# Kernel optimization log

Hardware: AMD Instinct MI355X
Metric: run time of the kernel (lower is better)

Reference implementation:

```python
import jax, jax.numpy as jnp
import numpy as np

B, S, H, NH, HD = 4, 4096, 1024, 16, 64

def setup_inputs() -> dict:
    key = jax.random.key(0)
    ks = jax.random.split(key, 5)
    scale = 1.0 / np.sqrt(H)
    return {
        "hidden_states": jax.random.normal(ks[0], (B, S, H), dtype=jnp.float32),
        "Wq": jax.random.normal(ks[1], (H, H), dtype=jnp.float32) * scale,
        "Wk": jax.random.normal(ks[2], (H, H), dtype=jnp.float32) * scale,
        "Wv": jax.random.normal(ks[3], (H, H), dtype=jnp.float32) * scale,
        "Wo": jax.random.normal(ks[4], (H, H), dtype=jnp.float32) * scale,
    }

def reference(hidden_states, Wq, Wk, Wv, Wo):
    b, s, h = hidden_states.shape
    # torch nn.Linear: y = x @ W.T
    q = (hidden_states @ Wq.T).reshape(b, s, NH, HD)
    k = (hidden_states @ Wk.T).reshape(b, s, NH, HD)
    v = (hidden_states @ Wv.T).reshape(b, s, NH, HD)
    # feature map: ELU (as in source, no +1)
    q = jax.nn.elu(q)
    k = jax.nn.elu(k)
    # per-head kv state: sum over sequence of outer products k_s v_s^T -> [b,h,d,e]
    kv = jnp.einsum('bshd,bshe->bhde', k, v)
    out = jnp.einsum('bqhd,bhde->bqhe', q, kv)  # [b,s,h,e]
    out = out.reshape(b, s, h)
    return out @ Wo.T  # dropout p=0.0 is identity
```

## Files before the change

### kernel.cpp

```cpp
#include <hip/hip_runtime.h>
#include <cstdint>
#include <cstddef>

#define B_  4
#define S_  4096
#define H_  1024
#define NH_ 16
#define M_  (B_*S_)

typedef __bf16 bf16x8 __attribute__((ext_vector_type(8)));
typedef float  f32x4  __attribute__((ext_vector_type(4)));

__device__ __forceinline__ unsigned short f2b(float f) {
  union { float f; unsigned u; } v; v.f = f;
  unsigned r = v.u + 0x7FFFu + ((v.u >> 16) & 1u);
  return (unsigned short)(r >> 16);
}
__device__ __forceinline__ float b2f(unsigned short u) {
  union { unsigned u; float f; } v; v.u = ((unsigned)u) << 16;
  return v.f;
}

#define GLD16(g, l) __builtin_amdgcn_global_load_lds( \
    (const __attribute__((address_space(1))) void*)(g), \
    (__attribute__((address_space(3))) void*)(l), 16, 0, 0)

#define VM0()  asm volatile("s_waitcnt vmcnt(0)" ::: "memory")
#define VM2()  asm volatile("s_waitcnt vmcnt(2)" ::: "memory")
#define BAR()  do { asm volatile("" ::: "memory"); __builtin_amdgcn_s_barrier(); \
                    asm volatile("" ::: "memory"); } while (0)

__global__ void cast_f32_bf16(const float* __restrict__ src,
                              unsigned short* __restrict__ dst, int n4) {
  int i = blockIdx.x * blockDim.x + threadIdx.x;
  if (i >= n4) return;
  float4 f = reinterpret_cast<const float4*>(src)[i];
  ushort4 o;
  o.x = f2b(f.x); o.y = f2b(f.y); o.z = f2b(f.z); o.w = f2b(f.w);
  reinterpret_cast<ushort4*>(dst)[i] = o;
}

__global__ void cast_w4(const float* __restrict__ w0, const float* __restrict__ w1,
                        const float* __restrict__ w2, const float* __restrict__ w3,
                        unsigned short* __restrict__ dst) {
  int i = blockIdx.x * blockDim.x + threadIdx.x;
  int w = i >> 18, j = i & 0x3FFFF;
  const float* src = (w == 0) ? w0 : (w == 1) ? w1 : (w == 2) ? w2 : w3;
  float4 f = reinterpret_cast<const float4*>(src)[j];
  ushort4 o;
  o.x = f2b(f.x); o.y = f2b(f.y); o.z = f2b(f.z); o.w = f2b(f.w);
  reinterpret_cast<ushort4*>(dst)[i] = o;
}

template<int MODE>
__global__ __launch_bounds__(512, 2) void gemm256(
    const unsigned short* __restrict__ A_,
    const unsigned short* __restrict__ Bt_,
    void* __restrict__ out) {
  __shared__ __align__(16) unsigned short LDS[2][2][16384];

  const int NTN = (MODE == 0) ? 12 : 4;
  const int nx  = gridDim.x >> 3;
  const int b2  = (blockIdx.x & 7) * nx + (blockIdx.x >> 3);
  const int tileM = (b2 / NTN) << 8;
  const int tileN = (b2 % NTN) << 8;

  const unsigned short* Bt_e =
      (MODE == 1) ? (Bt_ + ((size_t)(tileM >> 12) << 20)) : Bt_;

  const int tid  = threadIdx.x;
  const int lane = tid & 63, wv = tid >> 6;
  const int wmi  = wv >> 2;
  const int wni  = wv & 3;
  const int fr   = lane & 15, fq = lane >> 4;

  const int sr0 = tid >> 3,          sc0 = (tid & 7) ^ (sr0 & 7);
  const int sr1 = (tid + 512) >> 3,  sc1 = (tid & 7) ^ (sr1 & 7);

#define STG(NB, ARR, HM, SRC, RB, TT) do {                                      \
    GLD16((SRC) + (size_t)((RB) + (HM)*128 + sr0) * 1024 + (TT)*64 + sc0*8,     \
          &LDS[NB][ARR][(HM)*8192 + wv*512]);                                   \
    GLD16((SRC) + (size_t)((RB) + (HM)*128 + sr1) * 1024 + (TT)*64 + sc1*8,     \
          &LDS[NB][ARR][(HM)*8192 + 4096 + wv*512]);                            \
  } while (0)

#define READA(CB, MQ, DST) do {                                                 \
    _Pragma("unroll")                                                           \
    for (int m = 0; m < 4; m++) {                                               \
      int r = (MQ)*128 + wmi*64 + m*16 + fr;                                    \
      DST[m][0] = *(const bf16x8*)&LDS[CB][0][r*64 + ((fq    ) ^ (r&7))*8];     \
      DST[m][1] = *(const bf16x8*)&LDS[CB][0][r*64 + ((4 + fq) ^ (r&7))*8];     \
    }                                                                           \
  } while (0)

#define READB(CB, NQ, DST) do {                                                 \
    _Pragma("unroll")                                                           \
    for (int n = 0; n < 2; n++) {                                               \
      int r = (NQ)*128 + wni*32 + n*16 + fr;                                    \
      DST[n][0] = *(const bf16x8*)&LDS[CB][1][r*64 + ((fq    ) ^ (r&7))*8];     \
      DST[n][1] = *(const bf16x8*)&LDS[CB][1][r*64 + ((4 + fq) ^ (r&7))*8];     \
    }                                                                           \
  } while (0)

#define MMQ(MQ, NQ, AS, BS) do {                                                \
    __builtin_amdgcn_s_setprio(1);                                              \
    _Pragma("unroll")                                                           \
    for (int m = 0; m < 4; m++)                                                 \
      _Pragma("unroll")                                                         \
      for (int n = 0; n < 2; n++) {                                             \
        acc[MQ][NQ][m][n] = __builtin_amdgcn_mfma_f32_16x16x32_bf16(            \
            AS[m][0], BS[n][0], acc[MQ][NQ][m][n], 0, 0, 0);                    \
        acc[MQ][NQ][m][n] = __builtin_amdgcn_mfma_f32_16x16x32_bf16(            \
            AS[m][1], BS[n][1], acc[MQ][NQ][m][n], 0, 0, 0);                    \
      }                                                                         \
    __builtin_amdgcn_s_setprio(0);                                              \
  } while (0)

  f32x4 zero = {0.f, 0.f, 0.f, 0.f};
  f32x4 acc[2][2][4][2];
#pragma unroll
  for (int a = 0; a < 2; a++)
#pragma unroll
    for (int b = 0; b < 2; b++)
#pragma unroll
      for (int m = 0; m < 4; m++)
#pragma unroll
        for (int n = 0; n < 2; n++) acc[a][b][m][n] = zero;

  bf16x8 aA[4][2], aB[4][2], bA[2][2], bB[2][2];

  STG(0, 0, 0, A_,   tileM, 0);
  STG(0, 1, 0, Bt_e, tileN, 0);
  STG(0, 1, 1, Bt_e, tileN, 0);
  STG(0, 0, 1, A_,   tileM, 0);
  VM0();
  BAR();
  READA(0, 0, aA); READB(0, 0, bA);

  int cb = 0;
#pragma unroll 1
  for (int t = 0; t < 15; ++t) {
    const int nb = cb ^ 1;
    READB(cb, 1, bB);
    STG(nb, 0, 0, A_,   tileM, t + 1);
    VM2(); BAR();
    MMQ(0, 0, aA, bA);
    READA(cb, 1, aB);
    STG(nb, 1, 0, Bt_e, tileN, t + 1);
    BAR();
    MMQ(0, 1, aA, bB);
    STG(nb, 1, 1, Bt_e, tileN, t + 1);
    BAR();
    MMQ(1, 1, aB, bB);
    STG(nb, 0, 1, A_,   tileM, t + 1);
    VM2(); BAR();
    MMQ(1, 0, aB, bA);
    READA(nb, 0, aA); READB(nb, 0, bA);
    cb = nb;
  }
  READB(cb, 1, bB); VM0(); BAR();
  MMQ(0, 0, aA, bA);
  READA(cb, 1, aB); BAR();
  MMQ(0, 1, aA, bB);
  BAR();
  MMQ(1, 1, aB, bB);
  BAR();
  MMQ(1, 0, aB, bA);

  if (MODE == 0) {
    unsigned short* Ep = &LDS[0][0][0];
    const int reg = tileN >> 10;
    const bool doELU = (reg < 2);
    BAR();
#pragma unroll
    for (int mq = 0; mq < 2; mq++)
#pragma unroll
      for (int nq = 0; nq < 2; nq++)
#pragma unroll
        for (int m = 0; m < 4; m++)
#pragma unroll
          for (int n = 0; n < 2; n++)
#pragma unroll
            for (int r = 0; r < 4; r++) {
              int row = mq * 128 + wmi * 64 + m * 16 + fq * 4 + r;
              int col = nq * 128 + wni * 32 + n * 16 + fr;
              float v = acc[mq][nq][m][n][r];
              if (doELU) v = v > 0.f ? v : (expf(v) - 1.f);
              Ep[row * 256 + (col ^ ((row & 7) << 3))] = f2b(v);
            }
    BAR();
    unsigned short* outp = (unsigned short*)out + (size_t)reg * M_ * H_;
    const int lcbase = tileN & 1023;
#pragma unroll
    for (int it = 0; it < 16; it++) {
      int g = it * 512 + tid;
      int row = g >> 5, col = (g & 31) * 8;
      bf16x8 val = *(const bf16x8*)&Ep[row * 256 + (col ^ ((row & 7) << 3))];
      *(bf16x8*)&outp[(size_t)(tileM + row) * H_ + lcbase + col] = val;
    }
  } else {
    float* Ef = (float*)&LDS[0][0][0];
#pragma unroll
    for (int mq = 0; mq < 2; mq++) {
      BAR();
#pragma unroll
      for (int nq = 0; nq < 2; nq++)
#pragma unroll
        for (int m = 0; m < 4; m++)
#pragma unroll
          for (int n = 0; n < 2; n++)
#pragma unroll
            for (int r = 0; r < 4; r++) {
              int row = wmi * 64 + m * 16 + fq * 4 + r;
              int col = nq * 128 + wni * 32 + n * 16 + fr;
              Ef[row * 256 + (col ^ ((row & 7) << 2))] = acc[mq][nq][m][n][r];
            }
      BAR();
#pragma unroll
      for (int it = 0; it < 16; it++) {
        int g = it * 512 + tid;
        int row = g >> 6, c = (g & 63) * 4;
        f32x4 val = *(const f32x4*)&Ef[row * 256 + (c ^ ((row & 7) << 2))];
        *(f32x4*)&((float*)out)[(size_t)(tileM + mq * 128 + row) * H_ + tileN + c] = val;
      }
    }
  }
#undef MMQ
#undef READB
#undef READA
#undef STG
}

__global__ __launch_bounds__(256) void kv_partial(
    const unsigned short* __restrict__ Kb,
    const unsigned short* __restrict__ Vb,
    float* __restrict__ kvp) {
  __shared__ __align__(16) unsigned short kt[32 * 64];
  __shared__ __align__(16) unsigned short vt[32 * 64];
  const int bh = blockIdx.x >> 3;
  const int ch = blockIdx.x & 7;
  const int b  = bh >> 4, h = bh & 15;
  const int t  = threadIdx.x;
  const int rr = t >> 3;
  const int cc = (t & 7) * 8;
  const int d0 = (t >> 4) * 4;
  const int e0 = (t & 15) * 4;

  float acc[4][4] = {};
  for (int s0 = ch * 512; s0 < ch * 512 + 512; s0 += 32) {
    size_t g = (size_t)(b * S_ + s0 + rr) * H_ + h * 64 + cc;
    *reinterpret_cast<uint4*>(&kt[rr * 64 + cc]) = *reinterpret_cast<const uint4*>(Kb + g);
    *reinterpret_cast<uint4*>(&vt[rr * 64 + cc]) = *reinterpret_cast<const uint4*>(Vb + g);
    __syncthreads();
#pragma unroll 4
    for (int ss = 0; ss < 32; ss++) {
      ushort4 k4 = *reinterpret_cast<const ushort4*>(&kt[ss * 64 + d0]);
      ushort4 v4 = *reinterpret_cast<const ushort4*>(&vt[ss * 64 + e0]);
      float kf[4] = {b2f(k4.x), b2f(k4.y), b2f(k4.z), b2f(k4.w)};
      float vf[4] = {b2f(v4.x), b2f(v4.y), b2f(v4.z), b2f(v4.w)};
#pragma unroll
      for (int i = 0; i < 4; i++)
#pragma unroll
        for (int j = 0; j < 4; j++) acc[i][j] += kf[i] * vf[j];
    }
    __syncthreads();
  }
  float* outp = kvp + (size_t)blockIdx.x * 4096;
#pragma unroll
  for (int i = 0; i < 4; i++)
#pragma unroll
    for (int j = 0; j < 4; j++) outp[(d0 + i) * 64 + e0 + j] = acc[i][j];
}

__global__ __launch_bounds__(256) void kv_reduce(
    const float* __restrict__ kvp, unsigned short* __restrict__ KVb) {
  const int bh = blockIdx.x;
#pragma unroll
  for (int i = 0; i < 16; i++) {
    int idx = threadIdx.x + i * 256;
    float s = 0.f;
#pragma unroll
    for (int ch = 0; ch < 8; ch++) s += kvp[(size_t)(bh * 8 + ch) * 4096 + idx];
    KVb[(size_t)bh * 4096 + idx] = f2b(s);
  }
}

__global__ __launch_bounds__(256) void merge_m(
    const unsigned short* __restrict__ KVb,
    const unsigned short* __restrict__ Wob,
    unsigned short* __restrict__ MbT) {
  const int bh = blockIdx.x >> 2;
  const int nc = blockIdx.x & 3;
  const int b  = bh >> 4, h = bh & 15;
  const int lane = threadIdx.x & 63, wv = threadIdx.x >> 6;
  const int fr = lane & 15, fq = lane >> 4;
  const int ncb = nc * 256 + wv * 64;

  f32x4 zero = {0.f, 0.f, 0.f, 0.f};
  f32x4 acc[4][4];
#pragma unroll
  for (int i = 0; i < 4; i++)
#pragma unroll
    for (int j = 0; j < 4; j++) acc[i][j] = zero;

#pragma unroll
  for (int kk = 0; kk < 2; kk++) {
    bf16x8 af[4], bvv[4];
#pragma unroll
    for (int i = 0; i < 4; i++)
      af[i] = *(const bf16x8*)&KVb[(size_t)bh * 4096 + (i * 16 + fr) * 64 + kk * 32 + fq * 8];
#pragma unroll
    for (int j = 0; j < 4; j++)
      bvv[j] = *(const bf16x8*)&Wob[(size_t)(ncb + j * 16 + fr) * 1024 + h * 64 + kk * 32 + fq * 8];
#pragma unroll
    for (int i = 0; i < 4; i++)
#pragma unroll
      for (int j = 0; j < 4; j++)
        acc[i][j] = __builtin_amdgcn_mfma_f32_16x16x32_bf16(af[i], bvv[j], acc[i][j], 0, 0, 0);
  }
#pragma unroll
  for (int i = 0; i < 4; i++)
#pragma unroll
    for (int j = 0; j < 4; j++)
#pragma unroll
      for (int r = 0; r < 4; r++) {
        int n = ncb + j * 16 + fr;
        int k = h * 64 + i * 16 + fq * 4 + r;
        MbT[((size_t)b << 20) + (size_t)n * 1024 + k] = f2b(acc[i][j][r]);
      }
}

extern "C" void kernel_launch(void* const* d_in, const int* in_sizes, int n_in,
                              void* d_out, int out_size, void* d_ws, size_t ws_size,
                              hipStream_t stream) {
  (void)in_sizes; (void)n_in; (void)out_size; (void)ws_size;
  const float* X  = (const float*)d_in[0];
  const float* Wq = (const float*)d_in[1];
  const float* Wk = (const float*)d_in[2];
  const float* Wv = (const float*)d_in[3];
  const float* Wo = (const float*)d_in[4];

  char*  ws  = (char*)d_ws;
  size_t off = 0;
  auto alloc = [&](size_t bytes) -> char* {
    char* p = ws + off;
    off += (bytes + 255) & ~(size_t)255;
    return p;
  };
  unsigned short* Xb   = (unsigned short*)alloc((size_t)M_ * H_ * 2);
  unsigned short* Wcat = (unsigned short*)alloc((size_t)4 * H_ * H_ * 2);
  unsigned short* QKVb = (unsigned short*)alloc((size_t)3 * M_ * H_ * 2);
  float*          kvp  = (float*)alloc((size_t)64 * 8 * 4096 * 4);
  unsigned short* KVb  = (unsigned short*)alloc((size_t)64 * 4096 * 2);
  unsigned short* MbT  = (unsigned short*)alloc((size_t)4 * H_ * H_ * 2);

  unsigned short* Qb = QKVb;
  unsigned short* Kb = QKVb + (size_t)M_ * H_;
  unsigned short* Vb = QKVb + (size_t)2 * M_ * H_;
  unsigned short* Wob = Wcat + (size_t)3 * H_ * H_;

  cast_f32_bf16<<<(M_ * H_) / 1024, 256, 0, stream>>>(X, Xb, (M_ * H_) / 4);
  cast_w4<<<(4 * H_ * H_) / 1024, 256, 0, stream>>>(Wq, Wk, Wv, Wo, Wcat);

  gemm256<0><<<768, 512, 0, stream>>>(Xb, Wcat, QKVb);

  kv_partial<<<512, 256, 0, stream>>>(Kb, Vb, kvp);
  kv_reduce<<<64, 256, 0, stream>>>(kvp, KVb);
  merge_m<<<256, 256, 0, stream>>>(KVb, Wob, MbT);

  gemm256<1><<<256, 512, 0, stream>>>(Qb, MbT, (float*)d_out);
}
```

Measured before the change: 265.4 us.

## Restructure GEMM pipeline with per-warp-half LDS quadrants and deeper B prefetch

Reorganizes the GEMM LDS buffers into half-tile quadrants so each warp row/column group reads only its own 128-row half, which changes the warp-to-output mapping to contiguous 128x64 blocks per wave. The main loop now runs all 16 K-steps with staggered staging: A is loaded one step ahead and B two steps ahead into the buffer just freed, using vmcnt(4) waits. This is meant to hide global-load latency better and remove the peeled epilogue iteration. In exchange it adds barriers around every MFMA quarter, and the epilogue index mapping had to be rewritten to match the new layout.

```diff
diff --git a/kernel.cpp b/kernel.cpp
--- a/kernel.cpp
+++ b/kernel.cpp
@@ -26,7 +26,7 @@
     (__attribute__((address_space(3))) void*)(l), 16, 0, 0)
 
 #define VM0()  asm volatile("s_waitcnt vmcnt(0)" ::: "memory")
-#define VM2()  asm volatile("s_waitcnt vmcnt(2)" ::: "memory")
+#define VM4()  asm volatile("s_waitcnt vmcnt(4)" ::: "memory")
 #define BAR()  do { asm volatile("" ::: "memory"); __builtin_amdgcn_s_barrier(); \
                     asm volatile("" ::: "memory"); } while (0)
 
@@ -57,7 +57,7 @@
     const unsigned short* __restrict__ A_,
     const unsigned short* __restrict__ Bt_,
     void* __restrict__ out) {
-  __shared__ __align__(16) unsigned short LDS[2][2][16384];
+  __shared__ __align__(16) unsigned short LDS[2][2][2][8192];
 
   const int NTN = (MODE == 0) ? 12 : 4;
   const int nx  = gridDim.x >> 3;
@@ -72,33 +72,34 @@
   const int lane = tid & 63, wv = tid >> 6;
   const int wmi  = wv >> 2;
   const int wni  = wv & 3;
+  const int hb   = wni >> 1;
   const int fr   = lane & 15, fq = lane >> 4;
 
   const int sr0 = tid >> 3,          sc0 = (tid & 7) ^ (sr0 & 7);
   const int sr1 = (tid + 512) >> 3,  sc1 = (tid & 7) ^ (sr1 & 7);
 
-#define STG(NB, ARR, HM, SRC, RB, TT) do {                                      \
+#define STG(DB, ARR, HM, SRC, RB, TT) do {                                      \
     GLD16((SRC) + (size_t)((RB) + (HM)*128 + sr0) * 1024 + (TT)*64 + sc0*8,     \
-          &LDS[NB][ARR][(HM)*8192 + wv*512]);                                   \
+          &LDS[DB][ARR][HM][wv*512]);                                           \
     GLD16((SRC) + (size_t)((RB) + (HM)*128 + sr1) * 1024 + (TT)*64 + sc1*8,     \
-          &LDS[NB][ARR][(HM)*8192 + 4096 + wv*512]);                            \
+          &LDS[DB][ARR][HM][4096 + wv*512]);                                    \
   } while (0)
 
-#define READA(CB, MQ, DST) do {                                                 \
+#define RDA(CB, MQ, DST) do {                                                   \
     _Pragma("unroll")                                                           \
     for (int m = 0; m < 4; m++) {                                               \
-      int r = (MQ)*128 + wmi*64 + m*16 + fr;                                    \
-      DST[m][0] = *(const bf16x8*)&LDS[CB][0][r*64 + ((fq    ) ^ (r&7))*8];     \
-      DST[m][1] = *(const bf16x8*)&LDS[CB][0][r*64 + ((4 + fq) ^ (r&7))*8];     \
+      int rr = (MQ)*64 + m*16 + fr;                                             \
+      DST[m][0] = *(const bf16x8*)&LDS[CB][0][wmi][rr*64 + ((fq   ) ^ (rr&7))*8];\
+      DST[m][1] = *(const bf16x8*)&LDS[CB][0][wmi][rr*64 + ((4+fq ) ^ (rr&7))*8];\
     }                                                                           \
   } while (0)
 
-#define READB(CB, NQ, DST) do {                                                 \
+#define RDB(CB, NQ, DST) do {                                                   \
     _Pragma("unroll")                                                           \
     for (int n = 0; n < 2; n++) {                                               \
-      int r = (NQ)*128 + wni*32 + n*16 + fr;                                    \
-      DST[n][0] = *(const bf16x8*)&LDS[CB][1][r*64 + ((fq    ) ^ (r&7))*8];     \
-      DST[n][1] = *(const bf16x8*)&LDS[CB][1][r*64 + ((4 + fq) ^ (r&7))*8];     \
+      int rb = (wni & 1)*64 + (NQ)*32 + n*16 + fr;                              \
+      DST[n][0] = *(const bf16x8*)&LDS[CB][1][hb][rb*64 + ((fq   ) ^ (rb&7))*8];\
+      DST[n][1] = *(const bf16x8*)&LDS[CB][1][hb][rb*64 + ((4+fq ) ^ (rb&7))*8];\
     }                                                                           \
   } while (0)
 
@@ -119,59 +120,48 @@
   f32x4 zero = {0.f, 0.f, 0.f, 0.f};
   f32x4 acc[2][2][4][2];
 #pragma unroll
-  for (int a = 0; a < 2; a++)
-#pragma unroll
-    for (int b = 0; b < 2; b++)
+  for (int p = 0; p < 2; p++)
+#pragma unroll
+    for (int q = 0; q < 2; q++)
 #pragma unroll
       for (int m = 0; m < 4; m++)
 #pragma unroll
-        for (int n = 0; n < 2; n++) acc[a][b][m][n] = zero;
-
-  bf16x8 aA[4][2], aB[4][2], bA[2][2], bB[2][2];
+        for (int n = 0; n < 2; n++) acc[p][q][m][n] = zero;
+
+  bf16x8 a0[4][2], a1[4][2], b0[2][2], b1[2][2];
 
   STG(0, 0, 0, A_,   tileM, 0);
+  STG(0, 0, 1, A_,   tileM, 0);
   STG(0, 1, 0, Bt_e, tileN, 0);
   STG(0, 1, 1, Bt_e, tileN, 0);
-  STG(0, 0, 1, A_,   tileM, 0);
-  VM0();
+  STG(1, 1, 0, Bt_e, tileN, 1);
+  STG(1, 1, 1, Bt_e, tileN, 1);
+  VM4();
   BAR();
-  READA(0, 0, aA); READB(0, 0, bA);
 
   int cb = 0;
 #pragma unroll 1
-  for (int t = 0; t < 15; ++t) {
+  for (int t = 0; t < 16; ++t) {
     const int nb = cb ^ 1;
-    READB(cb, 1, bB);
-    STG(nb, 0, 0, A_,   tileM, t + 1);
-    VM2(); BAR();
-    MMQ(0, 0, aA, bA);
-    READA(cb, 1, aB);
-    STG(nb, 1, 0, Bt_e, tileN, t + 1);
-    BAR();
-    MMQ(0, 1, aA, bB);
-    STG(nb, 1, 1, Bt_e, tileN, t + 1);
-    BAR();
-    MMQ(1, 1, aB, bB);
-    STG(nb, 0, 1, A_,   tileM, t + 1);
-    VM2(); BAR();
-    MMQ(1, 0, aB, bA);
-    READA(nb, 0, aA); READB(nb, 0, bA);
+    RDA(cb, 0, a0); RDB(cb, 0, b0);
+    if (t + 1 < 16) STG(nb, 0, 0, A_, tileM, t + 1);
+    BAR(); MMQ(0, 0, a0, b0); BAR();
+    RDB(cb, 1, b1);
+    if (t + 1 < 16) STG(nb, 0, 1, A_, tileM, t + 1);
+    BAR(); MMQ(0, 1, a0, b1); BAR();
+    RDA(cb, 1, a1);
+    if (t + 2 < 16) STG(cb, 1, 0, Bt_e, tileN, t + 2);
+    BAR(); MMQ(1, 1, a1, b1); BAR();
+    if (t + 2 < 16) { STG(cb, 1, 1, Bt_e, tileN, t + 2); VM4(); }
+    else if (t + 1 < 16) { VM0(); }
+    BAR(); MMQ(1, 0, a1, b0); BAR();
     cb = nb;
   }
-  READB(cb, 1, bB); VM0(); BAR();
-  MMQ(0, 0, aA, bA);
-  READA(cb, 1, aB); BAR();
-  MMQ(0, 1, aA, bB);
-  BAR();
-  MMQ(1, 1, aB, bB);
-  BAR();
-  MMQ(1, 0, aB, bA);
 
   if (MODE == 0) {
-    unsigned short* Ep = &LDS[0][0][0];
+    unsigned short* Ep = &LDS[0][0][0][0];
     const int reg = tileN >> 10;
     const bool doELU = (reg < 2);
-    BAR();
 #pragma unroll
     for (int mq = 0; mq < 2; mq++)
 #pragma unroll
@@ -182,8 +172,8 @@
           for (int n = 0; n < 2; n++)
 #pragma unroll
             for (int r = 0; r < 4; r++) {
-              int row = mq * 128 + wmi * 64 + m * 16 + fq * 4 + r;
-              int col = nq * 128 + wni * 32 + n * 16 + fr;
+              int row = wmi * 128 + mq * 64 + m * 16 + fq * 4 + r;
+              int col = wni * 64 + nq * 32 + n * 16 + fr;
               float v = acc[mq][nq][m][n][r];
               if (doELU) v = v > 0.f ? v : (expf(v) - 1.f);
               Ep[row * 256 + (col ^ ((row & 7) << 3))] = f2b(v);
@@ -199,35 +189,39 @@
       *(bf16x8*)&outp[(size_t)(tileM + row) * H_ + lcbase + col] = val;
     }
   } else {
-    float* Ef = (float*)&LDS[0][0][0];
-#pragma unroll
-    for (int mq = 0; mq < 2; mq++) {
+    float* Ef = (float*)&LDS[0][0][0][0];
+#pragma unroll
+    for (int h = 0; h < 2; h++) {
       BAR();
-#pragma unroll
-      for (int nq = 0; nq < 2; nq++)
-#pragma unroll
-        for (int m = 0; m < 4; m++)
-#pragma unroll
-          for (int n = 0; n < 2; n++)
-#pragma unroll
-            for (int r = 0; r < 4; r++) {
-              int row = wmi * 64 + m * 16 + fq * 4 + r;
-              int col = nq * 128 + wni * 32 + n * 16 + fr;
-              Ef[row * 256 + (col ^ ((row & 7) << 2))] = acc[mq][nq][m][n][r];
-            }
+      if (wmi == h) {
+#pragma unroll
+        for (int mq = 0; mq < 2; mq++)
+#pragma unroll
+          for (int nq = 0; nq < 2; nq++)
+#pragma unroll
+            for (int m = 0; m < 4; m++)
+#pragma unroll
+              for (int n = 0; n < 2; n++)
+#pragma unroll
+                for (int r = 0; r < 4; r++) {
+                  int lr  = mq * 64 + m * 16 + fq * 4 + r;
+                  int col = wni * 64 + nq * 32 + n * 16 + fr;
+                  Ef[lr * 256 + (col ^ ((lr & 7) << 2))] = acc[mq][nq][m][n][r];
+                }
+      }
       BAR();
 #pragma unroll
       for (int it = 0; it < 16; it++) {
         int g = it * 512 + tid;
         int row = g >> 6, c = (g & 63) * 4;
         f32x4 val = *(const f32x4*)&Ef[row * 256 + (c ^ ((row & 7) << 2))];
-        *(f32x4*)&((float*)out)[(size_t)(tileM + mq * 128 + row) * H_ + tileN + c] = val;
+        *(f32x4*)&((float*)out)[(size_t)(tileM + h * 128 + row) * H_ + tileN + c] = val;
       }
     }
   }
 #undef MMQ
-#undef READB
-#undef READA
+#undef RDB
+#undef RDA
 #undef STG
 }
 
```

Result: no change. 266.2 us (+0.3%).
